# Performance work log

Hardware: AMD Instinct MI355X
Metric: run time of the kernel (lower is better)

Reference implementation:

```python
import jax, jax.numpy as jnp
import numpy as np

NODE_DIM, EDGE_DIM, HIDDEN = 1, 2, 64
N_NODES, N_EDGES = 50000, 1000000
MASK_FILL = -1e9


def setup_inputs() -> dict:
    key = jax.random.key(0)
    ks = jax.random.split(key, 10)
    x = jax.random.normal(ks[0], (N_NODES, NODE_DIM), dtype=jnp.float32)
    edge_index = jax.random.randint(ks[1], (2, N_EDGES), 0, N_NODES, dtype=jnp.int64)
    edge_attr = jax.random.normal(ks[2], (N_EDGES, EDGE_DIM), dtype=jnp.float32)
    edge_mask = jax.random.randint(ks[3], (N_EDGES,), 0, 2) > 0
    fin = 2 * NODE_DIM + EDGE_DIM  # 4
    s1 = 1.0 / np.sqrt(fin)
    s2 = 1.0 / np.sqrt(HIDDEN)
    W1 = jax.random.uniform(ks[4], (fin, HIDDEN), jnp.float32, -s1, s1)
    b1 = jax.random.uniform(ks[5], (HIDDEN,), jnp.float32, -s1, s1)
    W2 = jax.random.uniform(ks[6], (HIDDEN, HIDDEN), jnp.float32, -s2, s2)
    b2 = jax.random.uniform(ks[7], (HIDDEN,), jnp.float32, -s2, s2)
    Ws = jax.random.uniform(ks[8], (HIDDEN, 1), jnp.float32, -s2, s2)
    bs = jax.random.uniform(ks[9], (1,), jnp.float32, -s2, s2)
    return {"x": x, "edge_index": edge_index, "edge_attr": edge_attr,
            "edge_mask": edge_mask, "W1": W1, "b1": b1, "W2": W2, "b2": b2,
            "Ws": Ws, "bs": bs}


def reference(x, edge_index, edge_attr, edge_mask, W1, b1, W2, b2, Ws, bs):
    row, col = edge_index[0], edge_index[1]
    # gather src/dst node features and concat with edge_attr -> [E, 4]
    edge_input = jnp.concatenate([x[row], x[col], edge_attr], axis=1)
    h = jax.nn.relu(edge_input @ W1 + b1)   # [E, H]
    edge_emb = h @ W2 + b2                   # [E, H]
    scores = (edge_emb @ Ws + bs)[:, 0]      # [E]
    scores = jnp.where(edge_mask, scores, jnp.float32(MASK_FILL))
    return scores
```

## Files before the change

### kernel.cpp

```cpp
#include <hip/hip_runtime.h>

typedef float f2 __attribute__((ext_vector_type(2)));
typedef float f4 __attribute__((ext_vector_type(4)));
typedef int   i4 __attribute__((ext_vector_type(4)));

#define HIDDEN 64
#define MASK_FILL -1e9f
#define EPT 4

__global__ __launch_bounds__(256) void edge_score_fused(
    const float* __restrict__ x,
    const int* __restrict__ edge_index,
    const float* __restrict__ edge_attr,
    const int* __restrict__ edge_mask,
    const float* __restrict__ W1,
    const float* __restrict__ b1,
    const float* __restrict__ W2,
    const float* __restrict__ b2,
    const float* __restrict__ Ws,
    const float* __restrict__ bs,
    float* __restrict__ out, int E)
{
    __shared__ f4 bvS[32];
    __shared__ float cS;

    const int t = threadIdx.x;

    {
        const f4* W2v = reinterpret_cast<const f4*>(W2 + t * 16);
        const int j0 = 16 * (t & 3);
        float p = 0.f;
#pragma unroll
        for (int i = 0; i < 4; ++i) {
            const f4 wv = W2v[i];
            const int j = j0 + 4 * i;
            p = fmaf(wv.x, Ws[j], p);
            p = fmaf(wv.y, Ws[j + 1], p);
            p = fmaf(wv.z, Ws[j + 2], p);
            p = fmaf(wv.w, Ws[j + 3], p);
        }
        p += __shfl_xor(p, 1);
        p += __shfl_xor(p, 2);
        if ((t & 3) == 0) {
            const int k = t >> 2;
            reinterpret_cast<float*>(&bvS[k >> 1])[2 + (k & 1)] = p;
        }
    }
    if (t >= 64 && t < 128) {
        const int l = t - 64;
        float p = b2[l] * Ws[l];
#pragma unroll
        for (int off = 1; off < 64; off <<= 1) p += __shfl_xor(p, off);
        if (l == 0) cS = p + bs[0];
    } else if (t >= 192) {
        const int k = t - 192;
        reinterpret_cast<float*>(&bvS[k >> 1])[k & 1] = b1[k];
    }
    __syncthreads();

    const int tid = blockIdx.x * 256 + t;
    const int e = tid * EPT;
    if (e >= E) return;

    const i4 rows = *reinterpret_cast<const i4*>(edge_index + e);
    const i4 cols = *reinterpret_cast<const i4*>(edge_index + E + e);
    const i4 mk   = *reinterpret_cast<const i4*>(edge_mask + e);
    const f4 eaA  = *reinterpret_cast<const f4*>(edge_attr + 2 * e);
    const f4 eaB  = *reinterpret_cast<const f4*>(edge_attr + 2 * e + 4);

    const f2 xr0 = {x[rows.x], x[rows.x]}, xr1 = {x[rows.y], x[rows.y]},
             xr2 = {x[rows.z], x[rows.z]}, xr3 = {x[rows.w], x[rows.w]};
    const f2 xc0 = {x[cols.x], x[cols.x]}, xc1 = {x[cols.y], x[cols.y]},
             xc2 = {x[cols.z], x[cols.z]}, xc3 = {x[cols.w], x[cols.w]};
    const f2 e00 = {eaA.x, eaA.x}, e10 = {eaA.y, eaA.y};
    const f2 e01 = {eaA.z, eaA.z}, e11 = {eaA.w, eaA.w};
    const f2 e02 = {eaB.x, eaB.x}, e12 = {eaB.y, eaB.y};
    const f2 e03 = {eaB.z, eaB.z}, e13 = {eaB.w, eaB.w};

    const float c = cS;
    const f2 z2 = {0.f, 0.f};
    f2 a0 = {c, 0.f}, a1 = {c, 0.f}, a2 = {c, 0.f}, a3 = {c, 0.f};

#pragma unroll 4
    for (int k2 = 0; k2 < 32; ++k2) {
        const f2 w0 = {W1[2 * k2],       W1[2 * k2 + 1]};
        const f2 w1 = {W1[64 + 2 * k2],  W1[64 + 2 * k2 + 1]};
        const f2 w2 = {W1[128 + 2 * k2], W1[128 + 2 * k2 + 1]};
        const f2 w3 = {W1[192 + 2 * k2], W1[192 + 2 * k2 + 1]};
        const f4 C = bvS[k2];
        const f2 bb = {C.x, C.y}, vv = {C.z, C.w};

        f2 h0 = __builtin_elementwise_fma(xr0, w0, __builtin_elementwise_fma(xc0, w1,
                __builtin_elementwise_fma(e00, w2, __builtin_elementwise_fma(e10, w3, bb))));
        f2 h1 = __builtin_elementwise_fma(xr1, w0, __builtin_elementwise_fma(xc1, w1,
                __builtin_elementwise_fma(e01, w2, __builtin_elementwise_fma(e11, w3, bb))));
        f2 h2 = __builtin_elementwise_fma(xr2, w0, __builtin_elementwise_fma(xc2, w1,
                __builtin_elementwise_fma(e02, w2, __builtin_elementwise_fma(e12, w3, bb))));
        f2 h3 = __builtin_elementwise_fma(xr3, w0, __builtin_elementwise_fma(xc3, w1,
                __builtin_elementwise_fma(e03, w2, __builtin_elementwise_fma(e13, w3, bb))));
        a0 = __builtin_elementwise_fma(__builtin_elementwise_max(h0, z2), vv, a0);
        a1 = __builtin_elementwise_fma(__builtin_elementwise_max(h1, z2), vv, a1);
        a2 = __builtin_elementwise_fma(__builtin_elementwise_max(h2, z2), vv, a2);
        a3 = __builtin_elementwise_fma(__builtin_elementwise_max(h3, z2), vv, a3);
    }

    f4 res;
    res.x = mk.x ? (a0.x + a0.y) : MASK_FILL;
    res.y = mk.y ? (a1.x + a1.y) : MASK_FILL;
    res.z = mk.z ? (a2.x + a2.y) : MASK_FILL;
    res.w = mk.w ? (a3.x + a3.y) : MASK_FILL;
    *reinterpret_cast<f4*>(out + e) = res;
}

extern "C" void kernel_launch(void* const* d_in, const int* in_sizes, int n_in,
                              void* d_out, int out_size, void* d_ws, size_t ws_size,
                              hipStream_t stream) {
    const float* x          = (const float*)d_in[0];
    const int*   edge_index = (const int*)d_in[1];
    const float* edge_attr  = (const float*)d_in[2];
    const int*   edge_mask  = (const int*)d_in[3];
    const float* W1 = (const float*)d_in[4];
    const float* b1 = (const float*)d_in[5];
    const float* W2 = (const float*)d_in[6];
    const float* b2 = (const float*)d_in[7];
    const float* Ws = (const float*)d_in[8];
    const float* bs = (const float*)d_in[9];
    float* out = (float*)d_out;

    const int E = out_size;
    const int threads = 256;
    const int work = (E + EPT - 1) / EPT;
    const int blocks = (work + threads - 1) / threads;
    edge_score_fused<<<blocks, threads, 0, stream>>>(
        x, edge_index, edge_attr, edge_mask, W1, b1, W2, b2, Ws, bs, out, E);
}
```

Baseline: 19.42 us.

## Stage node features into LDS as bf16 and process eight edges per thread

Each 512-thread block copies the whole node-feature table into shared memory as bf16, then serves the row and column gathers from LDS instead of global memory. Each thread handles two groups of four edges, and the edge loads are issued before the staging loop so their latency overlaps it. This aims to cut random global-gather latency. In exchange, every block re-reads and converts the full 50000-node table, and the roughly 100KB of LDS per block limits residency to about one block per CU. x is also rounded to bf16, which loses precision, and the node count is hardcoded.

Measured after the change: 20.30 us. 4.5% more time.

```diff
diff --git a/kernel.cpp b/kernel.cpp
--- a/kernel.cpp
+++ b/kernel.cpp
@@ -3,12 +3,25 @@
 typedef float f2 __attribute__((ext_vector_type(2)));
 typedef float f4 __attribute__((ext_vector_type(4)));
 typedef int   i4 __attribute__((ext_vector_type(4)));
+typedef unsigned short u16x4 __attribute__((ext_vector_type(4)));
 
 #define HIDDEN 64
 #define MASK_FILL -1e9f
+#define NODES 50000
+#define TPB 512
 #define EPT 4
+#define EPB (TPB * EPT * 2)
 
-__global__ __launch_bounds__(256) void edge_score_fused(
+static __device__ __forceinline__ unsigned short f2bf(float f) {
+    unsigned u = __builtin_bit_cast(unsigned, f);
+    u += 0x7FFFu + ((u >> 16) & 1u);
+    return (unsigned short)(u >> 16);
+}
+static __device__ __forceinline__ float bf2f(unsigned short s) {
+    return __builtin_bit_cast(float, ((unsigned)s) << 16);
+}
+
+__global__ __launch_bounds__(TPB) void edge_score_fused(
     const float* __restrict__ x,
     const int* __restrict__ edge_index,
     const float* __restrict__ edge_attr,
@@ -21,12 +34,37 @@
     const float* __restrict__ bs,
     float* __restrict__ out, int E)
 {
+    __shared__ __align__(16) unsigned short xs[NODES];
     __shared__ f4 bvS[32];
     __shared__ float cS;
 
     const int t = threadIdx.x;
+    const int base = blockIdx.x * EPB;
+    if (base >= E) return;
 
-    {
+    const int eA = base + t * EPT;
+    const int eB = base + TPB * EPT + t * EPT;
+    const int ecA = eA < E ? eA : 0;
+    const int ecB = eB < E ? eB : 0;
+
+    const i4 rA = *reinterpret_cast<const i4*>(edge_index + ecA);
+    const i4 cA = *reinterpret_cast<const i4*>(edge_index + E + ecA);
+    const i4 mA = *reinterpret_cast<const i4*>(edge_mask + ecA);
+    const f4 aA = *reinterpret_cast<const f4*>(edge_attr + 2 * ecA);
+    const f4 zA = *reinterpret_cast<const f4*>(edge_attr + 2 * ecA + 4);
+    const i4 rB = *reinterpret_cast<const i4*>(edge_index + ecB);
+    const i4 cB = *reinterpret_cast<const i4*>(edge_index + E + ecB);
+    const i4 mB = *reinterpret_cast<const i4*>(edge_mask + ecB);
+    const f4 aB = *reinterpret_cast<const f4*>(edge_attr + 2 * ecB);
+    const f4 zB = *reinterpret_cast<const f4*>(edge_attr + 2 * ecB + 4);
+
+    for (int i = t; i < NODES / 4; i += TPB) {
+        const f4 v = reinterpret_cast<const f4*>(x)[i];
+        u16x4 u = { f2bf(v.x), f2bf(v.y), f2bf(v.z), f2bf(v.w) };
+        *reinterpret_cast<u16x4*>(&xs[i * 4]) = u;
+    }
+
+    if (t < 256) {
         const f4* W2v = reinterpret_cast<const f4*>(W2 + t * 16);
         const int j0 = 16 * (t & 3);
         float p = 0.f;
@@ -45,71 +83,69 @@
             const int k = t >> 2;
             reinterpret_cast<float*>(&bvS[k >> 1])[2 + (k & 1)] = p;
         }
-    }
-    if (t >= 64 && t < 128) {
-        const int l = t - 64;
+    } else if (t < 320) {
+        const int l = t - 256;
         float p = b2[l] * Ws[l];
 #pragma unroll
         for (int off = 1; off < 64; off <<= 1) p += __shfl_xor(p, off);
         if (l == 0) cS = p + bs[0];
-    } else if (t >= 192) {
-        const int k = t - 192;
+    } else if (t >= 448) {
+        const int k = t - 448;
         reinterpret_cast<float*>(&bvS[k >> 1])[k & 1] = b1[k];
     }
     __syncthreads();
 
-    const int tid = blockIdx.x * 256 + t;
-    const int e = tid * EPT;
-    if (e >= E) return;
+    const float c = cS;
 
-    const i4 rows = *reinterpret_cast<const i4*>(edge_index + e);
-    const i4 cols = *reinterpret_cast<const i4*>(edge_index + E + e);
-    const i4 mk   = *reinterpret_cast<const i4*>(edge_mask + e);
-    const f4 eaA  = *reinterpret_cast<const f4*>(edge_attr + 2 * e);
-    const f4 eaB  = *reinterpret_cast<const f4*>(edge_attr + 2 * e + 4);
+    auto compute_store = [&](const i4& rows, const i4& cols, const i4& mk,
+                             const f4& eaA, const f4& eaB, int e) {
+        const float g0 = bf2f(xs[rows.x]), g1 = bf2f(xs[rows.y]),
+                    g2 = bf2f(xs[rows.z]), g3 = bf2f(xs[rows.w]);
+        const float h0 = bf2f(xs[cols.x]), h1 = bf2f(xs[cols.y]),
+                    h2 = bf2f(xs[cols.z]), h3 = bf2f(xs[cols.w]);
+        const f2 xr0 = {g0, g0}, xr1 = {g1, g1}, xr2 = {g2, g2}, xr3 = {g3, g3};
+        const f2 xc0 = {h0, h0}, xc1 = {h1, h1}, xc2 = {h2, h2}, xc3 = {h3, h3};
+        const f2 e00 = {eaA.x, eaA.x}, e10 = {eaA.y, eaA.y};
+        const f2 e01 = {eaA.z, eaA.z}, e11 = {eaA.w, eaA.w};
+        const f2 e02 = {eaB.x, eaB.x}, e12 = {eaB.y, eaB.y};
+        const f2 e03 = {eaB.z, eaB.z}, e13 = {eaB.w, eaB.w};
 
-    const f2 xr0 = {x[rows.x], x[rows.x]}, xr1 = {x[rows.y], x[rows.y]},
-             xr2 = {x[rows.z], x[rows.z]}, xr3 = {x[rows.w], x[rows.w]};
-    const f2 xc0 = {x[cols.x], x[cols.x]}, xc1 = {x[cols.y], x[cols.y]},
-             xc2 = {x[cols.z], x[cols.z]}, xc3 = {x[cols.w], x[cols.w]};
-    const f2 e00 = {eaA.x, eaA.x}, e10 = {eaA.y, eaA.y};
-    const f2 e01 = {eaA.z, eaA.z}, e11 = {eaA.w, eaA.w};
-    const f2 e02 = {eaB.x, eaB.x}, e12 = {eaB.y, eaB.y};
-    const f2 e03 = {eaB.z, eaB.z}, e13 = {eaB.w, eaB.w};
-
-    const float c = cS;
-    const f2 z2 = {0.f, 0.f};
-    f2 a0 = {c, 0.f}, a1 = {c, 0.f}, a2 = {c, 0.f}, a3 = {c, 0.f};
+        const f2 z2 = {0.f, 0.f};
+        f2 a0 = {c, 0.f}, a1 = {c, 0.f}, a2 = {c, 0.f}, a3 = {c, 0.f};
 
 #pragma unroll 4
-    for (int k2 = 0; k2 < 32; ++k2) {
-        const f2 w0 = {W1[2 * k2],       W1[2 * k2 + 1]};
-        const f2 w1 = {W1[64 + 2 * k2],  W1[64 + 2 * k2 + 1]};
-        const f2 w2 = {W1[128 + 2 * k2], W1[128 + 2 * k2 + 1]};
-        const f2 w3 = {W1[192 + 2 * k2], W1[192 + 2 * k2 + 1]};
-        const f4 C = bvS[k2];
-        const f2 bb = {C.x, C.y}, vv = {C.z, C.w};
+        for (int k2 = 0; k2 < 32; ++k2) {
+            const f2 w0 = {W1[2 * k2],       W1[2 * k2 + 1]};
+            const f2 w1 = {W1[64 + 2 * k2],  W1[64 + 2 * k2 + 1]};
+            const f2 w2 = {W1[128 + 2 * k2], W1[128 + 2 * k2 + 1]};
+            const f2 w3 = {W1[192 + 2 * k2], W1[192 + 2 * k2 + 1]};
+            const f4 C = bvS[k2];
+            const f2 bb = {C.x, C.y}, vv = {C.z, C.w};
 
-        f2 h0 = __builtin_elementwise_fma(xr0, w0, __builtin_elementwise_fma(xc0, w1,
-                __builtin_elementwise_fma(e00, w2, __builtin_elementwise_fma(e10, w3, bb))));
-        f2 h1 = __builtin_elementwise_fma(xr1, w0, __builtin_elementwise_fma(xc1, w1,
-                __builtin_elementwise_fma(e01, w2, __builtin_elementwise_fma(e11, w3, bb))));
-        f2 h2 = __builtin_elementwise_fma(xr2, w0, __builtin_elementwise_fma(xc2, w1,
-                __builtin_elementwise_fma(e02, w2, __builtin_elementwise_fma(e12, w3, bb))));
-        f2 h3 = __builtin_elementwise_fma(xr3, w0, __builtin_elementwise_fma(xc3, w1,
-                __builtin_elementwise_fma(e03, w2, __builtin_elementwise_fma(e13, w3, bb))));
-        a0 = __builtin_elementwise_fma(__builtin_elementwise_max(h0, z2), vv, a0);
-        a1 = __builtin_elementwise_fma(__builtin_elementwise_max(h1, z2), vv, a1);
-        a2 = __builtin_elementwise_fma(__builtin_elementwise_max(h2, z2), vv, a2);
-        a3 = __builtin_elementwise_fma(__builtin_elementwise_max(h3, z2), vv, a3);
-    }
+            f2 q0 = __builtin_elementwise_fma(xr0, w0, __builtin_elementwise_fma(xc0, w1,
+                    __builtin_elementwise_fma(e00, w2, __builtin_elementwise_fma(e10, w3, bb))));
+            f2 q1 = __builtin_elementwise_fma(xr1, w0, __builtin_elementwise_fma(xc1, w1,
+                    __builtin_elementwise_fma(e01, w2, __builtin_elementwise_fma(e11, w3, bb))));
+            f2 q2 = __builtin_elementwise_fma(xr2, w0, __builtin_elementwise_fma(xc2, w1,
+                    __builtin_elementwise_fma(e02, w2, __builtin_elementwise_fma(e12, w3, bb))));
+            f2 q3 = __builtin_elementwise_fma(xr3, w0, __builtin_elementwise_fma(xc3, w1,
+                    __builtin_elementwise_fma(e03, w2, __builtin_elementwise_fma(e13, w3, bb))));
+            a0 = __builtin_elementwise_fma(__builtin_elementwise_max(q0, z2), vv, a0);
+            a1 = __builtin_elementwise_fma(__builtin_elementwise_max(q1, z2), vv, a1);
+            a2 = __builtin_elementwise_fma(__builtin_elementwise_max(q2, z2), vv, a2);
+            a3 = __builtin_elementwise_fma(__builtin_elementwise_max(q3, z2), vv, a3);
+        }
 
-    f4 res;
-    res.x = mk.x ? (a0.x + a0.y) : MASK_FILL;
-    res.y = mk.y ? (a1.x + a1.y) : MASK_FILL;
-    res.z = mk.z ? (a2.x + a2.y) : MASK_FILL;
-    res.w = mk.w ? (a3.x + a3.y) : MASK_FILL;
-    *reinterpret_cast<f4*>(out + e) = res;
+        f4 res;
+        res.x = mk.x ? (a0.x + a0.y) : MASK_FILL;
+        res.y = mk.y ? (a1.x + a1.y) : MASK_FILL;
+        res.z = mk.z ? (a2.x + a2.y) : MASK_FILL;
+        res.w = mk.w ? (a3.x + a3.y) : MASK_FILL;
+        if (e < E) *reinterpret_cast<f4*>(out + e) = res;
+    };
+
+    compute_store(rA, cA, mA, aA, zA, eA);
+    compute_store(rB, cB, mB, aB, zB, eB);
 }
 
 extern "C" void kernel_launch(void* const* d_in, const int* in_sizes, int n_in,
@@ -128,9 +164,7 @@
     float* out = (float*)d_out;
 
     const int E = out_size;
-    const int threads = 256;
-    const int work = (E + EPT - 1) / EPT;
-    const int blocks = (work + threads - 1) / threads;
-    edge_score_fused<<<blocks, threads, 0, stream>>>(
+    const int blocks = (E + EPB - 1) / EPB;
+    edge_score_fused<<<blocks, TPB, 0, stream>>>(
         x, edge_index, edge_attr, edge_mask, W1, b1, W2, b2, Ws, bs, out, E);
 }
```

## Process two edge chunks per thread and prefetch the second during the first

Applied to the files above, without the earlier changes.

Each thread now handles two groups of four edges, one grid-stride apart, and the grid is halved to match. The index, mask and attribute loads for the second group are issued before the first group's MLP loop, and scheduling barriers keep them there, so their memory latency overlaps with compute. Halving the block count also spreads the per-block shared-memory setup (the W2·Ws reduction and bias folding) over twice as many edges. The cost is more live registers, and the first chunk's write no longer has a bounds check, so it relies on E dividing cleanly.

Measured after the change: 19.98 us. 2.9% more time.

```diff
diff --git a/kernel.cpp b/kernel.cpp
--- a/kernel.cpp
+++ b/kernel.cpp
@@ -7,8 +7,57 @@
 #define HIDDEN 64
 #define MASK_FILL -1e9f
 #define EPT 4
+#define TPB 256
 
-__global__ __launch_bounds__(256) void edge_score_fused(
+__device__ __forceinline__ f4 kloop_compute(
+    const float* __restrict__ W1, const f4* bvS, float c,
+    const i4& rows, const i4& cols, const f4& eaA, const f4& eaB,
+    const i4& mk, const float* __restrict__ x)
+{
+    const f2 xr0 = {x[rows.x], x[rows.x]}, xr1 = {x[rows.y], x[rows.y]},
+             xr2 = {x[rows.z], x[rows.z]}, xr3 = {x[rows.w], x[rows.w]};
+    const f2 xc0 = {x[cols.x], x[cols.x]}, xc1 = {x[cols.y], x[cols.y]},
+             xc2 = {x[cols.z], x[cols.z]}, xc3 = {x[cols.w], x[cols.w]};
+    const f2 e00 = {eaA.x, eaA.x}, e10 = {eaA.y, eaA.y};
+    const f2 e01 = {eaA.z, eaA.z}, e11 = {eaA.w, eaA.w};
+    const f2 e02 = {eaB.x, eaB.x}, e12 = {eaB.y, eaB.y};
+    const f2 e03 = {eaB.z, eaB.z}, e13 = {eaB.w, eaB.w};
+
+    const f2 z2 = {0.f, 0.f};
+    f2 a0 = {c, 0.f}, a1 = {c, 0.f}, a2 = {c, 0.f}, a3 = {c, 0.f};
+
+#pragma unroll 4
+    for (int k2 = 0; k2 < 32; ++k2) {
+        const f2 w0 = {W1[2 * k2],       W1[2 * k2 + 1]};
+        const f2 w1 = {W1[64 + 2 * k2],  W1[64 + 2 * k2 + 1]};
+        const f2 w2 = {W1[128 + 2 * k2], W1[128 + 2 * k2 + 1]};
+        const f2 w3 = {W1[192 + 2 * k2], W1[192 + 2 * k2 + 1]};
+        const f4 C = bvS[k2];
+        const f2 bb = {C.x, C.y}, vv = {C.z, C.w};
+
+        f2 h0 = __builtin_elementwise_fma(xr0, w0, __builtin_elementwise_fma(xc0, w1,
+                __builtin_elementwise_fma(e00, w2, __builtin_elementwise_fma(e10, w3, bb))));
+        f2 h1 = __builtin_elementwise_fma(xr1, w0, __builtin_elementwise_fma(xc1, w1,
+                __builtin_elementwise_fma(e01, w2, __builtin_elementwise_fma(e11, w3, bb))));
+        f2 h2 = __builtin_elementwise_fma(xr2, w0, __builtin_elementwise_fma(xc2, w1,
+                __builtin_elementwise_fma(e02, w2, __builtin_elementwise_fma(e12, w3, bb))));
+        f2 h3 = __builtin_elementwise_fma(xr3, w0, __builtin_elementwise_fma(xc3, w1,
+                __builtin_elementwise_fma(e03, w2, __builtin_elementwise_fma(e13, w3, bb))));
+        a0 = __builtin_elementwise_fma(__builtin_elementwise_max(h0, z2), vv, a0);
+        a1 = __builtin_elementwise_fma(__builtin_elementwise_max(h1, z2), vv, a1);
+        a2 = __builtin_elementwise_fma(__builtin_elementwise_max(h2, z2), vv, a2);
+        a3 = __builtin_elementwise_fma(__builtin_elementwise_max(h3, z2), vv, a3);
+    }
+
+    f4 res;
+    res.x = mk.x ? (a0.x + a0.y) : MASK_FILL;
+    res.y = mk.y ? (a1.x + a1.y) : MASK_FILL;
+    res.z = mk.z ? (a2.x + a2.y) : MASK_FILL;
+    res.w = mk.w ? (a3.x + a3.y) : MASK_FILL;
+    return res;
+}
+
+__global__ __launch_bounds__(TPB) void edge_score_fused(
     const float* __restrict__ x,
     const int* __restrict__ edge_index,
     const float* __restrict__ edge_attr,
@@ -58,58 +107,72 @@
     }
     __syncthreads();
 
-    const int tid = blockIdx.x * 256 + t;
-    const int e = tid * EPT;
-    if (e >= E) return;
+    const float c = cS;
+    const int TOT4 = (int)gridDim.x * TPB * EPT;
+    const int e0 = (blockIdx.x * TPB + t) * EPT;
+    const int e1 = e0 + TOT4;
+    const bool v1 = e1 < E;
+    const int ec1 = v1 ? e1 : 0;
 
-    const i4 rows = *reinterpret_cast<const i4*>(edge_index + e);
-    const i4 cols = *reinterpret_cast<const i4*>(edge_index + E + e);
-    const i4 mk   = *reinterpret_cast<const i4*>(edge_mask + e);
-    const f4 eaA  = *reinterpret_cast<const f4*>(edge_attr + 2 * e);
-    const f4 eaB  = *reinterpret_cast<const f4*>(edge_attr + 2 * e + 4);
+    const i4 rows0 = *reinterpret_cast<const i4*>(edge_index + e0);
+    const i4 cols0 = *reinterpret_cast<const i4*>(edge_index + E + e0);
+    const i4 mk0   = *reinterpret_cast<const i4*>(edge_mask + e0);
+    const f4 eaA0  = *reinterpret_cast<const f4*>(edge_attr + 2 * e0);
+    const f4 eaB0  = *reinterpret_cast<const f4*>(edge_attr + 2 * e0 + 4);
 
-    const f2 xr0 = {x[rows.x], x[rows.x]}, xr1 = {x[rows.y], x[rows.y]},
-             xr2 = {x[rows.z], x[rows.z]}, xr3 = {x[rows.w], x[rows.w]};
-    const f2 xc0 = {x[cols.x], x[cols.x]}, xc1 = {x[cols.y], x[cols.y]},
-             xc2 = {x[cols.z], x[cols.z]}, xc3 = {x[cols.w], x[cols.w]};
-    const f2 e00 = {eaA.x, eaA.x}, e10 = {eaA.y, eaA.y};
-    const f2 e01 = {eaA.z, eaA.z}, e11 = {eaA.w, eaA.w};
-    const f2 e02 = {eaB.x, eaB.x}, e12 = {eaB.y, eaB.y};
-    const f2 e03 = {eaB.z, eaB.z}, e13 = {eaB.w, eaB.w};
+    const float g0 = x[rows0.x], g1 = x[rows0.y], g2 = x[rows0.z], g3 = x[rows0.w];
+    const float h0 = x[cols0.x], h1 = x[cols0.y], h2 = x[cols0.z], h3 = x[cols0.w];
+    asm volatile("" :: "v"(g0), "v"(g1), "v"(g2), "v"(g3),
+                       "v"(h0), "v"(h1), "v"(h2), "v"(h3));
+    __builtin_amdgcn_sched_barrier(0);
 
-    const float c = cS;
-    const f2 z2 = {0.f, 0.f};
-    f2 a0 = {c, 0.f}, a1 = {c, 0.f}, a2 = {c, 0.f}, a3 = {c, 0.f};
+    const i4 rows1 = *reinterpret_cast<const i4*>(edge_index + ec1);
+    const i4 cols1 = *reinterpret_cast<const i4*>(edge_index + E + ec1);
+    const i4 mk1   = *reinterpret_cast<const i4*>(edge_mask + ec1);
+    const f4 eaA1  = *reinterpret_cast<const f4*>(edge_attr + 2 * ec1);
+    const f4 eaB1  = *reinterpret_cast<const f4*>(edge_attr + 2 * ec1 + 4);
+    __builtin_amdgcn_sched_barrier(0);
 
+    {
+        const f2 xr0 = {g0, g0}, xr1 = {g1, g1}, xr2 = {g2, g2}, xr3 = {g3, g3};
+        const f2 xc0 = {h0, h0}, xc1 = {h1, h1}, xc2 = {h2, h2}, xc3 = {h3, h3};
+        const f2 e00 = {eaA0.x, eaA0.x}, e10 = {eaA0.y, eaA0.y};
+        const f2 e01 = {eaA0.z, eaA0.z}, e11 = {eaA0.w, eaA0.w};
+        const f2 e02 = {eaB0.x, eaB0.x}, e12 = {eaB0.y, eaB0.y};
+        const f2 e03 = {eaB0.z, eaB0.z}, e13 = {eaB0.w, eaB0.w};
+        const f2 z2 = {0.f, 0.f};
+        f2 a0 = {c, 0.f}, a1 = {c, 0.f}, a2 = {c, 0.f}, a3 = {c, 0.f};
 #pragma unroll 4
-    for (int k2 = 0; k2 < 32; ++k2) {
-        const f2 w0 = {W1[2 * k2],       W1[2 * k2 + 1]};
-        const f2 w1 = {W1[64 + 2 * k2],  W1[64 + 2 * k2 + 1]};
-        const f2 w2 = {W1[128 + 2 * k2], W1[128 + 2 * k2 + 1]};
-        const f2 w3 = {W1[192 + 2 * k2], W1[192 + 2 * k2 + 1]};
-        const f4 C = bvS[k2];
-        const f2 bb = {C.x, C.y}, vv = {C.z, C.w};
-
-        f2 h0 = __builtin_elementwise_fma(xr0, w0, __builtin_elementwise_fma(xc0, w1,
-                __builtin_elementwise_fma(e00, w2, __builtin_elementwise_fma(e10, w3, bb))));
-        f2 h1 = __builtin_elementwise_fma(xr1, w0, __builtin_elementwise_fma(xc1, w1,
-                __builtin_elementwise_fma(e01, w2, __builtin_elementwise_fma(e11, w3, bb))));
-        f2 h2 = __builtin_elementwise_fma(xr2, w0, __builtin_elementwise_fma(xc2, w1,
-                __builtin_elementwise_fma(e02, w2, __builtin_elementwise_fma(e12, w3, bb))));
-        f2 h3 = __builtin_elementwise_fma(xr3, w0, __builtin_elementwise_fma(xc3, w1,
-                __builtin_elementwise_fma(e03, w2, __builtin_elementwise_fma(e13, w3, bb))));
-        a0 = __builtin_elementwise_fma(__builtin_elementwise_max(h0, z2), vv, a0);
-        a1 = __builtin_elementwise_fma(__builtin_elementwise_max(h1, z2), vv, a1);
-        a2 = __builtin_elementwise_fma(__builtin_elementwise_max(h2, z2), vv, a2);
-        a3 = __builtin_elementwise_fma(__builtin_elementwise_max(h3, z2), vv, a3);
+        for (int k2 = 0; k2 < 32; ++k2) {
+            const f2 w0 = {W1[2 * k2],       W1[2 * k2 + 1]};
+            const f2 w1 = {W1[64 + 2 * k2],  W1[64 + 2 * k2 + 1]};
+            const f2 w2 = {W1[128 + 2 * k2], W1[128 + 2 * k2 + 1]};
+            const f2 w3 = {W1[192 + 2 * k2], W1[192 + 2 * k2 + 1]};
+            const f4 C = bvS[k2];
+            const f2 bb = {C.x, C.y}, vv = {C.z, C.w};
+            f2 q0 = __builtin_elementwise_fma(xr0, w0, __builtin_elementwise_fma(xc0, w1,
+                    __builtin_elementwise_fma(e00, w2, __builtin_elementwise_fma(e10, w3, bb))));
+            f2 q1 = __builtin_elementwise_fma(xr1, w0, __builtin_elementwise_fma(xc1, w1,
+                    __builtin_elementwise_fma(e01, w2, __builtin_elementwise_fma(e11, w3, bb))));
+            f2 q2 = __builtin_elementwise_fma(xr2, w0, __builtin_elementwise_fma(xc2, w1,
+                    __builtin_elementwise_fma(e02, w2, __builtin_elementwise_fma(e12, w3, bb))));
+            f2 q3 = __builtin_elementwise_fma(xr3, w0, __builtin_elementwise_fma(xc3, w1,
+                    __builtin_elementwise_fma(e03, w2, __builtin_elementwise_fma(e13, w3, bb))));
+            a0 = __builtin_elementwise_fma(__builtin_elementwise_max(q0, z2), vv, a0);
+            a1 = __builtin_elementwise_fma(__builtin_elementwise_max(q1, z2), vv, a1);
+            a2 = __builtin_elementwise_fma(__builtin_elementwise_max(q2, z2), vv, a2);
+            a3 = __builtin_elementwise_fma(__builtin_elementwise_max(q3, z2), vv, a3);
+        }
+        f4 res;
+        res.x = mk0.x ? (a0.x + a0.y) : MASK_FILL;
+        res.y = mk0.y ? (a1.x + a1.y) : MASK_FILL;
+        res.z = mk0.z ? (a2.x + a2.y) : MASK_FILL;
+        res.w = mk0.w ? (a3.x + a3.y) : MASK_FILL;
+        *reinterpret_cast<f4*>(out + e0) = res;
     }
 
-    f4 res;
-    res.x = mk.x ? (a0.x + a0.y) : MASK_FILL;
-    res.y = mk.y ? (a1.x + a1.y) : MASK_FILL;
-    res.z = mk.z ? (a2.x + a2.y) : MASK_FILL;
-    res.w = mk.w ? (a3.x + a3.y) : MASK_FILL;
-    *reinterpret_cast<f4*>(out + e) = res;
+    const f4 res1 = kloop_compute(W1, bvS, c, rows1, cols1, eaA1, eaB1, mk1, x);
+    if (v1) *reinterpret_cast<f4*>(out + e1) = res1;
 }
 
 extern "C" void kernel_launch(void* const* d_in, const int* in_sizes, int n_in,
@@ -128,9 +191,8 @@
     float* out = (float*)d_out;
 
     const int E = out_size;
-    const int threads = 256;
-    const int work = (E + EPT - 1) / EPT;
-    const int blocks = (work + threads - 1) / threads;
-    edge_score_fused<<<blocks, threads, 0, stream>>>(
+    const int stage_edges = (E + 1) / 2;
+    const int blocks = (stage_edges + TPB * EPT - 1) / (TPB * EPT);
+    edge_score_fused<<<blocks, TPB, 0, stream>>>(
         x, edge_index, edge_attr, edge_mask, W1, b1, W2, b2, Ws, bs, out, E);
 }
```
